# Kernel tuning notes

Hardware: AMD Instinct MI355X
Metric: run time of the kernel (lower is better)

The kernel has to match this reference:

```python
import jax, jax.numpy as jnp
import numpy as np

N_NODES = 100000


def gcn_conv(x, src, dst, W, b, n):
    # PyG GCNConv: add self-loops (weight 1), symmetric deg^-1/2 normalization,
    # linear transform, scatter-add to targets, then bias.
    loop = jnp.arange(n, dtype=src.dtype)
    s = jnp.concatenate([src, loop])
    d = jnp.concatenate([dst, loop])
    w = jnp.ones(s.shape[0], dtype=x.dtype)
    deg = jax.ops.segment_sum(w, d, num_segments=n)
    dis = jnp.where(deg > 0, jax.lax.rsqrt(deg), 0.0)
    norm = dis[s] * w * dis[d]                      # [E+N]
    h = x @ W                                       # [N, out]
    msg = h[s] * norm[:, None]                      # [E+N, out]
    out = jax.ops.segment_sum(msg, d, num_segments=n)
    return out + b


def setup_inputs() -> dict:
    key = jax.random.key(0)
    ks = jax.random.split(key, 8)
    num_node_types, emb_dim, hidden_dim, out_dim = 1000, 128, 128, 64
    n, e = N_NODES, 1600000
    x_node_types = jax.random.randint(ks[0], (n,), 0, num_node_types, dtype=jnp.int64 if jax.config.jax_enable_x64 else jnp.int32)
    edge_index = jax.random.randint(ks[1], (2, e), 0, n, dtype=x_node_types.dtype)
    emb = jax.random.normal(ks[2], (num_node_types, emb_dim), dtype=jnp.float32)
    W1 = jax.random.normal(ks[3], (emb_dim, hidden_dim), dtype=jnp.float32) / np.sqrt(emb_dim)
    b1 = jnp.zeros((hidden_dim,), dtype=jnp.float32)
    W2 = jax.random.normal(ks[4], (hidden_dim, out_dim), dtype=jnp.float32) / np.sqrt(hidden_dim)
    b2 = jnp.zeros((out_dim,), dtype=jnp.float32)
    return {"x_node_types": x_node_types, "edge_index": edge_index,
            "emb": emb, "W1": W1, "b1": b1, "W2": W2, "b2": b2}


def reference(x_node_types, edge_index, emb, W1, b1, W2, b2):
    n = N_NODES
    src, dst = edge_index[0], edge_index[1]
    x = emb[x_node_types]                           # embedding lookup [N, emb_dim]
    x = jax.nn.relu(gcn_conv(x, src, dst, W1, b1, n))
    # dropout p=0.5 is identity in eval mode (training=False)
    x = gcn_conv(x, src, dst, W2, b2, n)
    return x
```

## Files before the change

### kernel.cpp

```cpp
#include <hip/hip_runtime.h>
#include <hip/hip_bf16.h>


#define D1 128
#define D2 64
#define BSH 9
#define BW  512
#define BMAX 256
#define TILE 2048
#define SMASK 0x1FFFF

typedef __attribute__((ext_vector_type(8))) short short8v;
typedef __attribute__((ext_vector_type(4))) float f32x4;

__device__ __forceinline__ short bf16_hi(float x) {
    return (short)(__float_as_uint(x) >> 16);
}
__device__ __forceinline__ float hi_f(float x) {
    return __uint_as_float(__float_as_uint(x) & 0xFFFF0000u);
}
__device__ __forceinline__ short bf16_rne(float x) {
    unsigned u = __float_as_uint(x);
    return (short)((u + 0x7FFFu + ((u >> 16) & 1u)) >> 16);
}
__device__ __forceinline__ float bf16_f(unsigned short u) {
    return __uint_as_float((unsigned)u << 16);
}

__global__ __launch_bounds__(256) void bhist_k(const int* __restrict__ dst,
                                               int* __restrict__ bcnt, int e) {
    __shared__ int h[BMAX];
    if (threadIdx.x < BMAX) h[threadIdx.x] = 0;
    __syncthreads();
    int stride = gridDim.x * blockDim.x;
    for (int t = blockIdx.x * blockDim.x + threadIdx.x; t < e; t += stride)
        atomicAdd(&h[dst[t] >> BSH], 1);
    __syncthreads();
    if (threadIdx.x < BMAX && h[threadIdx.x])
        atomicAdd(&bcnt[threadIdx.x], h[threadIdx.x]);
}

__global__ void bscan_k(const int* __restrict__ bcnt, int* __restrict__ bbase,
                        int* __restrict__ bcur, int nb) {
    __shared__ int tmp[BMAX];
    int tid = threadIdx.x;
    int v = (tid < nb) ? bcnt[tid] : 0;
    tmp[tid] = v;
    __syncthreads();
    for (int s = 1; s < BMAX; s <<= 1) {
        int a = (tid >= s) ? tmp[tid - s] : 0;
        __syncthreads();
        tmp[tid] += a;
        __syncthreads();
    }
    if (tid < nb) { int ex = tmp[tid] - v; bbase[tid] = ex; bcur[tid] = ex; }
}

__global__ __launch_bounds__(256) void bpart_k(const int* __restrict__ src,
                                               const int* __restrict__ dst,
                                               int* __restrict__ bcur,
                                               unsigned* __restrict__ ebuf, int e) {
    __shared__ int hist[BMAX];
    __shared__ int chunk[BMAX];
    __shared__ int lcur[BMAX];
    int tid = threadIdx.x;
    int base = blockIdx.x * TILE;
    if (tid < BMAX) { hist[tid] = 0; lcur[tid] = 0; }
    __syncthreads();
    unsigned p8[8];
    int b8[8];
    #pragma unroll
    for (int i = 0; i < 8; ++i) {
        int t = base + i * 256 + tid;
        if (t < e) {
            int s = src[t], d = dst[t];
            b8[i] = d >> BSH;
            p8[i] = (unsigned)s | ((unsigned)(d & (BW - 1)) << 17);
            atomicAdd(&hist[b8[i]], 1);
        } else b8[i] = -1;
    }
    __syncthreads();
    if (tid < BMAX && hist[tid]) chunk[tid] = atomicAdd(&bcur[tid], hist[tid]);
    __syncthreads();
    #pragma unroll
    for (int i = 0; i < 8; ++i) {
        if (b8[i] >= 0) {
            int r = atomicAdd(&lcur[b8[i]], 1);
            ebuf[chunk[b8[i]] + r] = p8[i];
        }
    }
}

__global__ __launch_bounds__(512) void bcsr_count_k(const unsigned* __restrict__ ebuf,
                                                    const int* __restrict__ bbase,
                                                    const int* __restrict__ bcnt,
                                                    int* __restrict__ cnt,
                                                    int* __restrict__ off,
                                                    float* __restrict__ dis, int n) {
    __shared__ int lcnt[BW];
    __shared__ int lsc[BW];
    int b = blockIdx.x;
    int d0 = b << BSH;
    int tid = threadIdx.x;
    lcnt[tid] = 0;
    __syncthreads();
    int ebase = bbase[b], ecnt = bcnt[b];
    for (int t = tid; t < ecnt; t += BW)
        atomicAdd(&lcnt[ebuf[ebase + t] >> 17], 1);
    __syncthreads();
    int v = lcnt[tid];
    lsc[tid] = v;
    __syncthreads();
    for (int s = 1; s < BW; s <<= 1) {
        int a = (tid >= s) ? lsc[tid - s] : 0;
        __syncthreads();
        lsc[tid] += a;
        __syncthreads();
    }
    int node = d0 + tid;
    if (node < n) {
        cnt[node] = v;
        off[node] = ebase + lsc[tid] - v;
        dis[node] = rsqrtf((float)(v + 1));
    }
}

__global__ __launch_bounds__(512) void bcsr_fill_k(const unsigned* __restrict__ ebuf,
                                                   const int* __restrict__ bbase,
                                                   const int* __restrict__ bcnt,
                                                   const int* __restrict__ off,
                                                   const float* __restrict__ dis,
                                                   const int* __restrict__ types,
                                                   int2* __restrict__ csr_p, int n) {
    __shared__ int loff[BW];
    __shared__ float ldis[BW];
    __shared__ int lcur[BW];
    int b = blockIdx.x;
    int d0 = b << BSH;
    int tid = threadIdx.x;
    int node = d0 + tid;
    lcur[tid] = 0;
    if (node < n) { loff[tid] = off[node]; ldis[tid] = dis[node]; }
    __syncthreads();
    int ebase = bbase[b], ecnt = bcnt[b];
    for (int t = tid; t < ecnt; t += BW) {
        unsigned q = ebuf[ebase + t];
        int l = q >> 17;
        int s = q & SMASK;
        int r = atomicAdd(&lcur[l], 1);
        float coef = ldis[l] * dis[s];
        csr_p[loff[l] + r] = make_int2(s | (types[s] << 17), __float_as_int(coef));
    }
}

__global__ void w2prep_k(const float* __restrict__ W2,
                         short* __restrict__ w2h, short* __restrict__ w2l) {
    int t = blockIdx.x * blockDim.x + threadIdx.x;
    if (t >= D1 * D2) return;
    int k = t >> 6, c = t & 63;
    float v = W2[t];
    int ct = c >> 4, kb = k >> 5;
    int l = (((k >> 3) & 3) << 4) | (c & 15);
    int j = k & 7;
    int idx = (((ct << 2) | kb) * 64 + l) * 8 + j;
    w2h[idx] = bf16_hi(v);
    w2l[idx] = bf16_rne(v - hi_f(v));
}

__global__ __launch_bounds__(128) void gemm_emb_k(const float* __restrict__ emb,
                                                  const float* __restrict__ W1,
                                                  float* __restrict__ embW, int ntypes) {
    __shared__ float w[D1 * D1];
    for (int t = threadIdx.x; t < D1 * D1; t += 128) w[t] = W1[t];
    __syncthreads();
    int j = threadIdx.x;
    for (int r = blockIdx.x; r < ntypes; r += gridDim.x) {
        const float* er = emb + (size_t)r * D1;
        float acc = 0.f;
        #pragma unroll 8
        for (int k = 0; k < D1; ++k) acc = fmaf(er[k], w[k * D1 + j], acc);
        embW[(size_t)r * D1 + j] = acc;
    }
}

__global__ __launch_bounds__(256) void agg1_k(const int* __restrict__ types,
                                              const int2* __restrict__ csr_p,
                                              const int* __restrict__ off,
                                              const int* __restrict__ cnt,
                                              const float* __restrict__ dis,
                                              const float* __restrict__ embW,
                                              const float* __restrict__ b1,
                                              float* __restrict__ x1, int n) {
    int i = (blockIdx.x * blockDim.x + threadIdx.x) >> 6;
    if (i >= n) return;
    int lane = threadIdx.x & 63;
    int sub = lane >> 5;
    int fl = (lane & 31) << 2;
    float disi = dis[i];
    int base = off[i], c = cnt[i];
    int total = c + 1;
    float4 a0 = make_float4(0.f, 0.f, 0.f, 0.f);
    float4 a1 = make_float4(0.f, 0.f, 0.f, 0.f);
    for (int cbk = 0; cbk < total; cbk += 64) {
        int idx = cbk + lane;
        int t_l = 0;
        float c_l = 0.f;
        if (idx < c) {
            int2 q = csr_p[base + idx];
            t_l = q.x >> 17;
            c_l = __int_as_float(q.y);
        } else if (idx == c) {
            t_l = types[i];
            c_l = disi * disi;
        }
        int m = min(64, total - cbk);
        int k0 = 0;
        for (; k0 + 8 <= m; k0 += 8) {
            int   tA = __shfl(t_l, k0 + sub);
            float cA = __shfl(c_l, k0 + sub);
            int   tB = __shfl(t_l, k0 + 2 + sub);
            float cB = __shfl(c_l, k0 + 2 + sub);
            int   tC = __shfl(t_l, k0 + 4 + sub);
            float cC = __shfl(c_l, k0 + 4 + sub);
            int   tD = __shfl(t_l, k0 + 6 + sub);
            float cD = __shfl(c_l, k0 + 6 + sub);
            float4 vA = *(const float4*)(embW + (size_t)tA * D1 + fl);
            float4 vB = *(const float4*)(embW + (size_t)tB * D1 + fl);
            float4 vC = *(const float4*)(embW + (size_t)tC * D1 + fl);
            float4 vD = *(const float4*)(embW + (size_t)tD * D1 + fl);
            a0.x = fmaf(vA.x, cA, a0.x); a0.y = fmaf(vA.y, cA, a0.y);
            a0.z = fmaf(vA.z, cA, a0.z); a0.w = fmaf(vA.w, cA, a0.w);
            a1.x = fmaf(vB.x, cB, a1.x); a1.y = fmaf(vB.y, cB, a1.y);
            a1.z = fmaf(vB.z, cB, a1.z); a1.w = fmaf(vB.w, cB, a1.w);
            a0.x = fmaf(vC.x, cC, a0.x); a0.y = fmaf(vC.y, cC, a0.y);
            a0.z = fmaf(vC.z, cC, a0.z); a0.w = fmaf(vC.w, cC, a0.w);
            a1.x = fmaf(vD.x, cD, a1.x); a1.y = fmaf(vD.y, cD, a1.y);
            a1.z = fmaf(vD.z, cD, a1.z); a1.w = fmaf(vD.w, cD, a1.w);
        }
        for (; k0 < m; k0 += 2) {
            int k = k0 + sub;
            int   t = __shfl(t_l, k);
            float cf = __shfl(c_l, k);
            float4 v = *(const float4*)(embW + (size_t)t * D1 + fl);
            a0.x = fmaf(v.x, cf, a0.x); a0.y = fmaf(v.y, cf, a0.y);
            a0.z = fmaf(v.z, cf, a0.z); a0.w = fmaf(v.w, cf, a0.w);
        }
    }
    float4 acc = make_float4(a0.x + a1.x, a0.y + a1.y, a0.z + a1.z, a0.w + a1.w);
    acc.x += __shfl_xor(acc.x, 32);
    acc.y += __shfl_xor(acc.y, 32);
    acc.z += __shfl_xor(acc.z, 32);
    acc.w += __shfl_xor(acc.w, 32);
    if (sub == 0) {
        float4 bv = ((const float4*)b1)[lane & 31];
        acc.x = fmaxf(acc.x + bv.x, 0.f);
        acc.y = fmaxf(acc.y + bv.y, 0.f);
        acc.z = fmaxf(acc.z + bv.z, 0.f);
        acc.w = fmaxf(acc.w + bv.w, 0.f);
        ((float4*)(x1 + (size_t)i * D1))[lane & 31] = acc;
    }
}

__global__ __launch_bounds__(256) void gemm2_k(const float* __restrict__ x1,
                                               const short* __restrict__ w2h,
                                               const short* __restrict__ w2l,
                                               unsigned short* __restrict__ h2b, int n) {
    int gw = (blockIdx.x * blockDim.x + threadIdx.x) >> 6;
    int lane = threadIdx.x & 63;
    int r0 = gw << 4;
    if (r0 >= n) return;
    int row = r0 + (lane & 15);
    int kq = lane >> 4;
    bool ok = row < n;
    const float* xr = x1 + (size_t)row * D1 + kq * 8;
    short8v ah[4], al[4];
    #pragma unroll
    for (int kb = 0; kb < 4; ++kb) {
        float4 v0, v1;
        if (ok) {
            v0 = *(const float4*)(xr + kb * 32);
            v1 = *(const float4*)(xr + kb * 32 + 4);
        } else {
            v0 = make_float4(0.f, 0.f, 0.f, 0.f);
            v1 = v0;
        }
        float xv[8] = {v0.x, v0.y, v0.z, v0.w, v1.x, v1.y, v1.z, v1.w};
        #pragma unroll
        for (int j = 0; j < 8; ++j) {
            ah[kb][j] = bf16_hi(xv[j]);
            al[kb][j] = bf16_rne(xv[j] - hi_f(xv[j]));
        }
    }
    const short8v* w2hv = (const short8v*)w2h;
    const short8v* w2lv = (const short8v*)w2l;
    #pragma unroll
    for (int ct = 0; ct < 4; ++ct) {
        f32x4 acc = {0.f, 0.f, 0.f, 0.f};
        #pragma unroll
        for (int kb = 0; kb < 4; ++kb) {
            short8v bh = w2hv[(ct * 4 + kb) * 64 + lane];
            short8v bl = w2lv[(ct * 4 + kb) * 64 + lane];
            acc = __builtin_amdgcn_mfma_f32_16x16x32_bf16(ah[kb], bh, acc, 0, 0, 0);
            acc = __builtin_amdgcn_mfma_f32_16x16x32_bf16(al[kb], bh, acc, 0, 0, 0);
            acc = __builtin_amdgcn_mfma_f32_16x16x32_bf16(ah[kb], bl, acc, 0, 0, 0);
        }
        #pragma unroll
        for (int v = 0; v < 4; ++v) {
            int orow = r0 + (lane >> 4) * 4 + v;
            if (orow < n)
                h2b[(size_t)orow * D2 + ct * 16 + (lane & 15)] =
                    (unsigned short)bf16_rne(acc[v]);
        }
    }
}

__global__ __launch_bounds__(256) void agg2_k(const int2* __restrict__ csr_p,
                                              const int* __restrict__ off,
                                              const int* __restrict__ cnt,
                                              const float* __restrict__ dis,
                                              const unsigned short* __restrict__ h2b,
                                              const float* __restrict__ b2,
                                              float* __restrict__ out, int n) {
    int i = (blockIdx.x * blockDim.x + threadIdx.x) >> 6;
    if (i >= n) return;
    int lane = threadIdx.x & 63;
    int sub = lane >> 4;
    int fl = (lane & 15) << 2;
    float disi = dis[i];
    int base = off[i], c = cnt[i];
    int total = c + 1;
    float4 a0 = make_float4(0.f, 0.f, 0.f, 0.f);
    float4 a1 = make_float4(0.f, 0.f, 0.f, 0.f);
    for (int cbk = 0; cbk < total; cbk += 64) {
        int idx = cbk + lane;
        int s_l = i;
        float c_l = 0.f;
        if (idx < c) {
            int2 q = csr_p[base + idx];
            s_l = q.x & SMASK;
            c_l = __int_as_float(q.y);
        } else if (idx == c) {
            c_l = disi * disi;
        }
        int m = min(64, total - cbk);
        int k0 = 0;
        for (; k0 + 16 <= m; k0 += 16) {
            int   sA = __shfl(s_l, k0 + sub);
            float cA = __shfl(c_l, k0 + sub);
            int   sB = __shfl(s_l, k0 + 4 + sub);
            float cB = __shfl(c_l, k0 + 4 + sub);
            int   sC = __shfl(s_l, k0 + 8 + sub);
            float cC = __shfl(c_l, k0 + 8 + sub);
            int   sD = __shfl(s_l, k0 + 12 + sub);
            float cD = __shfl(c_l, k0 + 12 + sub);
            ushort4 hA = *(const ushort4*)(h2b + (size_t)sA * D2 + fl);
            ushort4 hB = *(const ushort4*)(h2b + (size_t)sB * D2 + fl);
            ushort4 hC = *(const ushort4*)(h2b + (size_t)sC * D2 + fl);
            ushort4 hD = *(const ushort4*)(h2b + (size_t)sD * D2 + fl);
            a0.x = fmaf(bf16_f(hA.x), cA, a0.x); a0.y = fmaf(bf16_f(hA.y), cA, a0.y);
            a0.z = fmaf(bf16_f(hA.z), cA, a0.z); a0.w = fmaf(bf16_f(hA.w), cA, a0.w);
            a1.x = fmaf(bf16_f(hB.x), cB, a1.x); a1.y = fmaf(bf16_f(hB.y), cB, a1.y);
            a1.z = fmaf(bf16_f(hB.z), cB, a1.z); a1.w = fmaf(bf16_f(hB.w), cB, a1.w);
            a0.x = fmaf(bf16_f(hC.x), cC, a0.x); a0.y = fmaf(bf16_f(hC.y), cC, a0.y);
            a0.z = fmaf(bf16_f(hC.z), cC, a0.z); a0.w = fmaf(bf16_f(hC.w), cC, a0.w);
            a1.x = fmaf(bf16_f(hD.x), cD, a1.x); a1.y = fmaf(bf16_f(hD.y), cD, a1.y);
            a1.z = fmaf(bf16_f(hD.z), cD, a1.z); a1.w = fmaf(bf16_f(hD.w), cD, a1.w);
        }
        for (; k0 < m; k0 += 4) {
            int k = k0 + sub;
            int   s = __shfl(s_l, k);
            float cf = __shfl(c_l, k);
            ushort4 hv = *(const ushort4*)(h2b + (size_t)s * D2 + fl);
            a0.x = fmaf(bf16_f(hv.x), cf, a0.x); a0.y = fmaf(bf16_f(hv.y), cf, a0.y);
            a0.z = fmaf(bf16_f(hv.z), cf, a0.z); a0.w = fmaf(bf16_f(hv.w), cf, a0.w);
        }
    }
    float4 acc = make_float4(a0.x + a1.x, a0.y + a1.y, a0.z + a1.z, a0.w + a1.w);
    acc.x += __shfl_xor(acc.x, 16);
    acc.y += __shfl_xor(acc.y, 16);
    acc.z += __shfl_xor(acc.z, 16);
    acc.w += __shfl_xor(acc.w, 16);
    acc.x += __shfl_xor(acc.x, 32);
    acc.y += __shfl_xor(acc.y, 32);
    acc.z += __shfl_xor(acc.z, 32);
    acc.w += __shfl_xor(acc.w, 32);
    if (sub == 0) {
        float4 bv = ((const float4*)b2)[lane & 15];
        acc.x += bv.x;
        acc.y += bv.y;
        acc.z += bv.z;
        acc.w += bv.w;
        ((float4*)(out + (size_t)i * D2))[lane & 15] = acc;
    }
}

extern "C" void kernel_launch(void* const* d_in, const int* in_sizes, int n_in,
                              void* d_out, int out_size, void* d_ws, size_t ws_size,
                              hipStream_t stream) {
    const int* types = (const int*)d_in[0];
    const int* edges = (const int*)d_in[1];
    const float* emb = (const float*)d_in[2];
    const float* W1  = (const float*)d_in[3];
    const float* b1  = (const float*)d_in[4];
    const float* W2  = (const float*)d_in[5];
    const float* b2  = (const float*)d_in[6];
    float* out = (float*)d_out;

    const int n = in_sizes[0];
    const int e = in_sizes[1] / 2;
    const int ntypes = in_sizes[2] / D1;
    const int* src = edges;
    const int* dst = edges + e;
    const int nb = (n + BW - 1) >> BSH;

    char* p = (char*)d_ws;
    auto alloc = [&](size_t bytes) {
        char* r = p;
        p += (bytes + 255) & ~(size_t)255;
        return r;
    };
    int*      bcnt  = (int*)      alloc(BMAX * 4);
    int*      bbase = (int*)      alloc(BMAX * 4);
    int*      bcur  = (int*)      alloc(BMAX * 4);
    int*      cnt   = (int*)      alloc((size_t)n * 4);
    int*      off   = (int*)      alloc((size_t)n * 4);
    float*    dis   = (float*)    alloc((size_t)n * 4);
    short*    w2h   = (short*)    alloc((size_t)D1 * D2 * 2);
    short*    w2l   = (short*)    alloc((size_t)D1 * D2 * 2);
    unsigned* ebuf  = (unsigned*) alloc((size_t)e * 4);
    int2*     csr_p = (int2*)     alloc((size_t)e * 8);
    float*    embW  = (float*)    alloc((size_t)ntypes * D1 * 4);
    float*    x1    = (float*)    alloc((size_t)n * D1 * 4);
    unsigned short* h2b = (unsigned short*)alloc((size_t)n * D2 * 2);
    (void)ws_size;

    hipMemsetAsync(bcnt, 0, BMAX * 4, stream);

    bhist_k<<<512, 256, 0, stream>>>(dst, bcnt, e);
    bscan_k<<<1, BMAX, 0, stream>>>(bcnt, bbase, bcur, nb);
    bpart_k<<<(e + TILE - 1) / TILE, 256, 0, stream>>>(src, dst, bcur, ebuf, e);
    bcsr_count_k<<<nb, BW, 0, stream>>>(ebuf, bbase, bcnt, cnt, off, dis, n);
    bcsr_fill_k<<<nb, BW, 0, stream>>>(ebuf, bbase, bcnt, off, dis, types, csr_p, n);
    w2prep_k<<<(D1 * D2 + 255) / 256, 256, 0, stream>>>(W2, w2h, w2l);

    gemm_emb_k<<<256, 128, 0, stream>>>(emb, W1, embW, ntypes);
    int nwb = (n + 3) / 4;
    agg1_k<<<nwb, 256, 0, stream>>>(types, csr_p, off, cnt, dis, embW, b1, x1, n);

    int ngw = (n + 15) / 16;
    gemm2_k<<<(ngw + 3) / 4, 256, 0, stream>>>(x1, w2h, w2l, h2b, n);
    agg2_k<<<nwb, 256, 0, stream>>>(csr_p, off, cnt, dis, h2b, b2, out, n);
}
```

Baseline: 283.2 us.

## Map four nodes per wavefront in aggregations and store embW as bf16

Both aggregation kernels now give each node a 16-lane quarter of a wavefront instead of a whole wavefront. Each quarter walks its own edge list two edges at a time, with no shuffles and no cross-lane reduction, until every quarter in the wave is done. The precomputed emb@W1 table is stored in bf16 instead of fp32, which halves the bytes fetched per gather in layer 1. The cost is divergence when degrees differ within a wave, narrower per-lane work, and extra rounding error from the bf16 table.

Measured after the change: 285.1 us. Within noise of the previous version (+0.7%).

```diff
diff --git a/kernel.cpp b/kernel.cpp
--- a/kernel.cpp
+++ b/kernel.cpp
@@ -11,6 +11,7 @@
 #define SMASK 0x1FFFF
 
 typedef __attribute__((ext_vector_type(8))) short short8v;
+typedef __attribute__((ext_vector_type(8))) unsigned short ushort8v;
 typedef __attribute__((ext_vector_type(4))) float f32x4;
 
 __device__ __forceinline__ short bf16_hi(float x) {
@@ -169,7 +170,8 @@
 
 __global__ __launch_bounds__(128) void gemm_emb_k(const float* __restrict__ emb,
                                                   const float* __restrict__ W1,
-                                                  float* __restrict__ embW, int ntypes) {
+                                                  unsigned short* __restrict__ embWb,
+                                                  int ntypes) {
     __shared__ float w[D1 * D1];
     for (int t = threadIdx.x; t < D1 * D1; t += 128) w[t] = W1[t];
     __syncthreads();
@@ -179,7 +181,7 @@
         float acc = 0.f;
         #pragma unroll 8
         for (int k = 0; k < D1; ++k) acc = fmaf(er[k], w[k * D1 + j], acc);
-        embW[(size_t)r * D1 + j] = acc;
+        embWb[(size_t)r * D1 + j] = (unsigned short)bf16_rne(acc);
     }
 }
 
@@ -188,76 +190,60 @@
                                               const int* __restrict__ off,
                                               const int* __restrict__ cnt,
                                               const float* __restrict__ dis,
-                                              const float* __restrict__ embW,
+                                              const unsigned short* __restrict__ embWb,
                                               const float* __restrict__ b1,
                                               float* __restrict__ x1, int n) {
-    int i = (blockIdx.x * blockDim.x + threadIdx.x) >> 6;
-    if (i >= n) return;
+    int gw = (blockIdx.x * blockDim.x + threadIdx.x) >> 6;
     int lane = threadIdx.x & 63;
-    int sub = lane >> 5;
-    int fl = (lane & 31) << 2;
-    float disi = dis[i];
-    int base = off[i], c = cnt[i];
+    int sub = lane >> 4;
+    int sl = lane & 15;
+    int i = gw * 4 + sub;
+    bool ok = i < n;
+    int ii = ok ? i : 0;
+    float disi = dis[ii];
+    int base = off[ii];
+    int c = ok ? cnt[ii] : -1;
     int total = c + 1;
+    int ti = types[ii];
     float4 a0 = make_float4(0.f, 0.f, 0.f, 0.f);
-    float4 a1 = make_float4(0.f, 0.f, 0.f, 0.f);
-    for (int cbk = 0; cbk < total; cbk += 64) {
-        int idx = cbk + lane;
-        int t_l = 0;
-        float c_l = 0.f;
-        if (idx < c) {
-            int2 q = csr_p[base + idx];
-            t_l = q.x >> 17;
-            c_l = __int_as_float(q.y);
-        } else if (idx == c) {
-            t_l = types[i];
-            c_l = disi * disi;
-        }
-        int m = min(64, total - cbk);
-        int k0 = 0;
-        for (; k0 + 8 <= m; k0 += 8) {
-            int   tA = __shfl(t_l, k0 + sub);
-            float cA = __shfl(c_l, k0 + sub);
-            int   tB = __shfl(t_l, k0 + 2 + sub);
-            float cB = __shfl(c_l, k0 + 2 + sub);
-            int   tC = __shfl(t_l, k0 + 4 + sub);
-            float cC = __shfl(c_l, k0 + 4 + sub);
-            int   tD = __shfl(t_l, k0 + 6 + sub);
-            float cD = __shfl(c_l, k0 + 6 + sub);
-            float4 vA = *(const float4*)(embW + (size_t)tA * D1 + fl);
-            float4 vB = *(const float4*)(embW + (size_t)tB * D1 + fl);
-            float4 vC = *(const float4*)(embW + (size_t)tC * D1 + fl);
-            float4 vD = *(const float4*)(embW + (size_t)tD * D1 + fl);
-            a0.x = fmaf(vA.x, cA, a0.x); a0.y = fmaf(vA.y, cA, a0.y);
-            a0.z = fmaf(vA.z, cA, a0.z); a0.w = fmaf(vA.w, cA, a0.w);
-            a1.x = fmaf(vB.x, cB, a1.x); a1.y = fmaf(vB.y, cB, a1.y);
-            a1.z = fmaf(vB.z, cB, a1.z); a1.w = fmaf(vB.w, cB, a1.w);
-            a0.x = fmaf(vC.x, cC, a0.x); a0.y = fmaf(vC.y, cC, a0.y);
-            a0.z = fmaf(vC.z, cC, a0.z); a0.w = fmaf(vC.w, cC, a0.w);
-            a1.x = fmaf(vD.x, cD, a1.x); a1.y = fmaf(vD.y, cD, a1.y);
-            a1.z = fmaf(vD.z, cD, a1.z); a1.w = fmaf(vD.w, cD, a1.w);
-        }
-        for (; k0 < m; k0 += 2) {
-            int k = k0 + sub;
-            int   t = __shfl(t_l, k);
-            float cf = __shfl(c_l, k);
-            float4 v = *(const float4*)(embW + (size_t)t * D1 + fl);
-            a0.x = fmaf(v.x, cf, a0.x); a0.y = fmaf(v.y, cf, a0.y);
-            a0.z = fmaf(v.z, cf, a0.z); a0.w = fmaf(v.w, cf, a0.w);
-        }
-    }
-    float4 acc = make_float4(a0.x + a1.x, a0.y + a1.y, a0.z + a1.z, a0.w + a1.w);
-    acc.x += __shfl_xor(acc.x, 32);
-    acc.y += __shfl_xor(acc.y, 32);
-    acc.z += __shfl_xor(acc.z, 32);
-    acc.w += __shfl_xor(acc.w, 32);
-    if (sub == 0) {
-        float4 bv = ((const float4*)b1)[lane & 31];
-        acc.x = fmaxf(acc.x + bv.x, 0.f);
-        acc.y = fmaxf(acc.y + bv.y, 0.f);
-        acc.z = fmaxf(acc.z + bv.z, 0.f);
-        acc.w = fmaxf(acc.w + bv.w, 0.f);
-        ((float4*)(x1 + (size_t)i * D1))[lane & 31] = acc;
+    float4 a1 = a0, a2 = a0, a3 = a0;
+    const unsigned short* ewb = embWb + (sl << 3);
+    for (int k0 = 0;; k0 += 2) {
+        bool act0 = k0 < total;
+        if (!__any(act0)) break;
+        bool act1 = k0 + 1 < total;
+        int tp0 = 0, tp1 = 0;
+        float c0 = 0.f, c1 = 0.f;
+        if (act0) {
+            if (k0 < c) { int2 q = csr_p[base + k0]; tp0 = q.x >> 17; c0 = __int_as_float(q.y); }
+            else        { tp0 = ti; c0 = disi * disi; }
+        }
+        if (act1) {
+            if (k0 + 1 < c) { int2 q = csr_p[base + k0 + 1]; tp1 = q.x >> 17; c1 = __int_as_float(q.y); }
+            else            { tp1 = ti; c1 = disi * disi; }
+        }
+        ushort8v r0 = *(const ushort8v*)(ewb + (size_t)tp0 * D1);
+        ushort8v r1 = *(const ushort8v*)(ewb + (size_t)tp1 * D1);
+        a0.x = fmaf(bf16_f(r0[0]), c0, a0.x); a0.y = fmaf(bf16_f(r0[1]), c0, a0.y);
+        a0.z = fmaf(bf16_f(r0[2]), c0, a0.z); a0.w = fmaf(bf16_f(r0[3]), c0, a0.w);
+        a1.x = fmaf(bf16_f(r0[4]), c0, a1.x); a1.y = fmaf(bf16_f(r0[5]), c0, a1.y);
+        a1.z = fmaf(bf16_f(r0[6]), c0, a1.z); a1.w = fmaf(bf16_f(r0[7]), c0, a1.w);
+        a2.x = fmaf(bf16_f(r1[0]), c1, a2.x); a2.y = fmaf(bf16_f(r1[1]), c1, a2.y);
+        a2.z = fmaf(bf16_f(r1[2]), c1, a2.z); a2.w = fmaf(bf16_f(r1[3]), c1, a2.w);
+        a3.x = fmaf(bf16_f(r1[4]), c1, a3.x); a3.y = fmaf(bf16_f(r1[5]), c1, a3.y);
+        a3.z = fmaf(bf16_f(r1[6]), c1, a3.z); a3.w = fmaf(bf16_f(r1[7]), c1, a3.w);
+    }
+    if (ok) {
+        float4 f0 = make_float4(a0.x + a2.x, a0.y + a2.y, a0.z + a2.z, a0.w + a2.w);
+        float4 f1 = make_float4(a1.x + a3.x, a1.y + a3.y, a1.z + a3.z, a1.w + a3.w);
+        float4 bv0 = ((const float4*)b1)[sl * 2];
+        float4 bv1 = ((const float4*)b1)[sl * 2 + 1];
+        f0.x = fmaxf(f0.x + bv0.x, 0.f); f0.y = fmaxf(f0.y + bv0.y, 0.f);
+        f0.z = fmaxf(f0.z + bv0.z, 0.f); f0.w = fmaxf(f0.w + bv0.w, 0.f);
+        f1.x = fmaxf(f1.x + bv1.x, 0.f); f1.y = fmaxf(f1.y + bv1.y, 0.f);
+        f1.z = fmaxf(f1.z + bv1.z, 0.f); f1.w = fmaxf(f1.w + bv1.w, 0.f);
+        ((float4*)(x1 + (size_t)i * D1))[sl * 2] = f0;
+        ((float4*)(x1 + (size_t)i * D1))[sl * 2 + 1] = f1;
     }
 }
 
@@ -321,76 +307,49 @@
                                               const unsigned short* __restrict__ h2b,
                                               const float* __restrict__ b2,
                                               float* __restrict__ out, int n) {
-    int i = (blockIdx.x * blockDim.x + threadIdx.x) >> 6;
-    if (i >= n) return;
+    int gw = (blockIdx.x * blockDim.x + threadIdx.x) >> 6;
     int lane = threadIdx.x & 63;
     int sub = lane >> 4;
-    int fl = (lane & 15) << 2;
-    float disi = dis[i];
-    int base = off[i], c = cnt[i];
+    int sl = lane & 15;
+    int i = gw * 4 + sub;
+    bool ok = i < n;
+    int ii = ok ? i : 0;
+    float disi = dis[ii];
+    int base = off[ii];
+    int c = ok ? cnt[ii] : -1;
     int total = c + 1;
     float4 a0 = make_float4(0.f, 0.f, 0.f, 0.f);
-    float4 a1 = make_float4(0.f, 0.f, 0.f, 0.f);
-    for (int cbk = 0; cbk < total; cbk += 64) {
-        int idx = cbk + lane;
-        int s_l = i;
-        float c_l = 0.f;
-        if (idx < c) {
-            int2 q = csr_p[base + idx];
-            s_l = q.x & SMASK;
-            c_l = __int_as_float(q.y);
-        } else if (idx == c) {
-            c_l = disi * disi;
-        }
-        int m = min(64, total - cbk);
-        int k0 = 0;
-        for (; k0 + 16 <= m; k0 += 16) {
-            int   sA = __shfl(s_l, k0 + sub);
-            float cA = __shfl(c_l, k0 + sub);
-            int   sB = __shfl(s_l, k0 + 4 + sub);
-            float cB = __shfl(c_l, k0 + 4 + sub);
-            int   sC = __shfl(s_l, k0 + 8 + sub);
-            float cC = __shfl(c_l, k0 + 8 + sub);
-            int   sD = __shfl(s_l, k0 + 12 + sub);
-            float cD = __shfl(c_l, k0 + 12 + sub);
-            ushort4 hA = *(const ushort4*)(h2b + (size_t)sA * D2 + fl);
-            ushort4 hB = *(const ushort4*)(h2b + (size_t)sB * D2 + fl);
-            ushort4 hC = *(const ushort4*)(h2b + (size_t)sC * D2 + fl);
-            ushort4 hD = *(const ushort4*)(h2b + (size_t)sD * D2 + fl);
-            a0.x = fmaf(bf16_f(hA.x), cA, a0.x); a0.y = fmaf(bf16_f(hA.y), cA, a0.y);
-            a0.z = fmaf(bf16_f(hA.z), cA, a0.z); a0.w = fmaf(bf16_f(hA.w), cA, a0.w);
-            a1.x = fmaf(bf16_f(hB.x), cB, a1.x); a1.y = fmaf(bf16_f(hB.y), cB, a1.y);
-            a1.z = fmaf(bf16_f(hB.z), cB, a1.z); a1.w = fmaf(bf16_f(hB.w), cB, a1.w);
-            a0.x = fmaf(bf16_f(hC.x), cC, a0.x); a0.y = fmaf(bf16_f(hC.y), cC, a0.y);
-            a0.z = fmaf(bf16_f(hC.z), cC, a0.z); a0.w = fmaf(bf16_f(hC.w), cC, a0.w);
-            a1.x = fmaf(bf16_f(hD.x), cD, a1.x); a1.y = fmaf(bf16_f(hD.y), cD, a1.y);
-            a1.z = fmaf(bf16_f(hD.z), cD, a1.z); a1.w = fmaf(bf16_f(hD.w), cD, a1.w);
-        }
-        for (; k0 < m; k0 += 4) {
-            int k = k0 + sub;
-            int   s = __shfl(s_l, k);
-            float cf = __shfl(c_l, k);
-            ushort4 hv = *(const ushort4*)(h2b + (size_t)s * D2 + fl);
-            a0.x = fmaf(bf16_f(hv.x), cf, a0.x); a0.y = fmaf(bf16_f(hv.y), cf, a0.y);
-            a0.z = fmaf(bf16_f(hv.z), cf, a0.z); a0.w = fmaf(bf16_f(hv.w), cf, a0.w);
-        }
-    }
-    float4 acc = make_float4(a0.x + a1.x, a0.y + a1.y, a0.z + a1.z, a0.w + a1.w);
-    acc.x += __shfl_xor(acc.x, 16);
-    acc.y += __shfl_xor(acc.y, 16);
-    acc.z += __shfl_xor(acc.z, 16);
-    acc.w += __shfl_xor(acc.w, 16);
-    acc.x += __shfl_xor(acc.x, 32);
-    acc.y += __shfl_xor(acc.y, 32);
-    acc.z += __shfl_xor(acc.z, 32);
-    acc.w += __shfl_xor(acc.w, 32);
-    if (sub == 0) {
-        float4 bv = ((const float4*)b2)[lane & 15];
-        acc.x += bv.x;
-        acc.y += bv.y;
-        acc.z += bv.z;
-        acc.w += bv.w;
-        ((float4*)(out + (size_t)i * D2))[lane & 15] = acc;
+    float4 a1 = a0;
+    const unsigned short* hb = h2b + (sl << 2);
+    for (int k0 = 0;; k0 += 2) {
+        bool act0 = k0 < total;
+        if (!__any(act0)) break;
+        bool act1 = k0 + 1 < total;
+        int s0 = 0, s1 = 0;
+        float c0 = 0.f, c1 = 0.f;
+        if (act0) {
+            if (k0 < c) { int2 q = csr_p[base + k0]; s0 = q.x & SMASK; c0 = __int_as_float(q.y); }
+            else        { s0 = ii; c0 = disi * disi; }
+        }
+        if (act1) {
+            if (k0 + 1 < c) { int2 q = csr_p[base + k0 + 1]; s1 = q.x & SMASK; c1 = __int_as_float(q.y); }
+            else            { s1 = ii; c1 = disi * disi; }
+        }
+        ushort4 r0 = *(const ushort4*)(hb + (size_t)s0 * D2);
+        ushort4 r1 = *(const ushort4*)(hb + (size_t)s1 * D2);
+        a0.x = fmaf(bf16_f(r0.x), c0, a0.x); a0.y = fmaf(bf16_f(r0.y), c0, a0.y);
+        a0.z = fmaf(bf16_f(r0.z), c0, a0.z); a0.w = fmaf(bf16_f(r0.w), c0, a0.w);
+        a1.x = fmaf(bf16_f(r1.x), c1, a1.x); a1.y = fmaf(bf16_f(r1.y), c1, a1.y);
+        a1.z = fmaf(bf16_f(r1.z), c1, a1.z); a1.w = fmaf(bf16_f(r1.w), c1, a1.w);
+    }
+    if (ok) {
+        float4 bv = ((const float4*)b2)[sl];
+        float4 f;
+        f.x = a0.x + a1.x + bv.x;
+        f.y = a0.y + a1.y + bv.y;
+        f.z = a0.z + a1.z + bv.z;
+        f.w = a0.w + a1.w + bv.w;
+        ((float4*)(out + (size_t)i * D2))[sl] = f;
     }
 }
 
@@ -429,7 +388,7 @@
     short*    w2l   = (short*)    alloc((size_t)D1 * D2 * 2);
     unsigned* ebuf  = (unsigned*) alloc((size_t)e * 4);
     int2*     csr_p = (int2*)     alloc((size_t)e * 8);
-    float*    embW  = (float*)    alloc((size_t)ntypes * D1 * 4);
+    unsigned short* embWb = (unsigned short*)alloc((size_t)ntypes * D1 * 2);
     float*    x1    = (float*)    alloc((size_t)n * D1 * 4);
     unsigned short* h2b = (unsigned short*)alloc((size_t)n * D2 * 2);
     (void)ws_size;
@@ -443,11 +402,11 @@
     bcsr_fill_k<<<nb, BW, 0, stream>>>(ebuf, bbase, bcnt, off, dis, types, csr_p, n);
     w2prep_k<<<(D1 * D2 + 255) / 256, 256, 0, stream>>>(W2, w2h, w2l);
 
-    gemm_emb_k<<<256, 128, 0, stream>>>(emb, W1, embW, ntypes);
-    int nwb = (n + 3) / 4;
-    agg1_k<<<nwb, 256, 0, stream>>>(types, csr_p, off, cnt, dis, embW, b1, x1, n);
+    gemm_emb_k<<<256, 128, 0, stream>>>(emb, W1, embWb, ntypes);
+    int ngrid = (n + 15) / 16;
+    agg1_k<<<ngrid, 256, 0, stream>>>(types, csr_p, off, cnt, dis, embWb, b1, x1, n);
 
     int ngw = (n + 15) / 16;
     gemm2_k<<<(ngw + 3) / 4, 256, 0, stream>>>(x1, w2h, w2l, h2b, n);
-    agg2_k<<<nwb, 256, 0, stream>>>(csr_p, off, cnt, dis, h2b, b2, out, n);
-}
+    agg2_k<<<ngrid, 256, 0, stream>>>(csr_p, off, cnt, dis, h2b, b2, out, n);
+}
```
